# Kernel optimization log

Hardware: AMD Instinct MI355X
Metric: run time of the kernel (lower is better)

Reference implementation:

```python
import jax, jax.numpy as jnp
import numpy as np

# Dims from HierarchicalDecoder defaults; NB is the torch batch size, which the
# original code accidentally uses as the LSTM time axis (2D input to nn.LSTM).
Z_DIM, U, COND, HID, OUT, NB = 512, 16, 512, 1024, 16, 512


def _unif(key, shape, scale):
    return jax.random.uniform(key, shape, jnp.float32, -scale, scale)


def setup_inputs() -> dict:
    key = jax.random.key(0)
    ks = jax.random.split(key, 20)
    d = Z_DIM // U            # 32
    sd = 1.0 / np.sqrt(d)
    sc = 1.0 / np.sqrt(COND)
    sh = 1.0 / np.sqrt(HID)
    return {
        "z": jax.random.normal(ks[0], (NB, Z_DIM), jnp.float32),
        "fc0_w": _unif(ks[1], (COND, d), sd), "fc0_b": _unif(ks[2], (COND,), sd),
        "fc1_w": _unif(ks[3], (HID, COND), sc), "fc1_b": _unif(ks[4], (HID,), sc),
        # conductor LSTM (2 layers, input=hidden=COND); b = b_ih + b_hh fused
        "c_wih0": _unif(ks[5], (4 * COND, COND), sc), "c_whh0": _unif(ks[6], (4 * COND, COND), sc), "c_b0": _unif(ks[7], (4 * COND,), sc),
        "c_wih1": _unif(ks[8], (4 * COND, COND), sc), "c_whh1": _unif(ks[9], (4 * COND, COND), sc), "c_b1": _unif(ks[10], (4 * COND,), sc),
        # decoder LSTM (2 layers, input COND->HID then HID->HID)
        "d_wih0": _unif(ks[11], (4 * HID, COND), sh), "d_whh0": _unif(ks[12], (4 * HID, HID), sh), "d_b0": _unif(ks[13], (4 * HID,), sh),
        "d_wih1": _unif(ks[14], (4 * HID, HID), sh), "d_whh1": _unif(ks[15], (4 * HID, HID), sh), "d_b1": _unif(ks[16], (4 * HID,), sh),
        "out_w": _unif(ks[17], (OUT, HID), sh), "out_b": _unif(ks[18], (OUT,), sh),
    }


def _lstm_layer(x, h0, c0, wih, whh, b):
    # x: [U, T, I]; h0, c0: [U, H]. PyTorch gate order: i, f, g, o.
    gx = jnp.einsum('uti,gi->utg', x, wih) + b  # input contribution, hoisted out of scan

    def step(carry, g):
        h, c = carry
        g = g + h @ whh.T
        i, f, gg, o = jnp.split(g, 4, axis=-1)
        c = jax.nn.sigmoid(f) * c + jax.nn.sigmoid(i) * jnp.tanh(gg)
        h = jax.nn.sigmoid(o) * jnp.tanh(c)
        return (h, c), h

    (hT, _), hs = jax.lax.scan(step, (h0, c0), jnp.swapaxes(gx, 0, 1))
    return jnp.swapaxes(hs, 0, 1), hT  # [U, T, H], [U, H]


def _forward(z, fc0_w, fc0_b, fc1_w, fc1_b, c_wih0, c_whh0, c_b0, c_wih1, c_whh1, c_b1,
             d_wih0, d_whh0, d_b0, d_wih1, d_whh1, d_b1, out_w, out_b):
    B = z.shape[0]
    # [U, B, z_dim//U]; the Python loop over U in the original is vectorized as a batch axis.
    x = jnp.swapaxes(z.reshape(B, U, -1), 0, 1)
    x = jnp.tanh(x @ fc0_w.T + fc0_b)  # fc0 -> [U, B, COND]; B is the LSTM time axis
    zC = jnp.zeros((U, COND), x.dtype)
    h0s, hT0 = _lstm_layer(x, zC, zC, c_wih0, c_whh0, c_b0)
    h1s, hT1 = _lstm_layer(h0s, zC, zC, c_wih1, c_whh1, c_b1)
    # fc1 on final conductor hidden of each layer -> decoder initial h; initial c = 0
    hd0 = jnp.tanh(hT0 @ fc1_w.T + fc1_b)
    hd1 = jnp.tanh(hT1 @ fc1_w.T + fc1_b)
    zH = jnp.zeros((U, HID), x.dtype)
    d0s, _ = _lstm_layer(h1s, hd0, zH, d_wih0, d_whh0, d_b0)
    d1s, _ = _lstm_layer(d0s, hd1, zH, d_wih1, d_whh1, d_b1)
    logits = d1s @ out_w.T + out_b                 # [U, B, OUT]
    probs = jax.nn.softmax(logits, axis=1)         # Softmax(dim=0) over the B axis per subsequence
    return jnp.swapaxes(probs, 0, 1).reshape(B, U * OUT)  # torch.cat(outputs, dim=1)


def reference(z, fc0_w, fc0_b, fc1_w, fc1_b, c_wih0, c_whh0, c_b0, c_wih1, c_whh1, c_b1,
              d_wih0, d_whh0, d_b0, d_wih1, d_whh1, d_b1, out_w, out_b):
    return _forward(z, fc0_w, fc0_b, fc1_w, fc1_b, c_wih0, c_whh0, c_b0, c_wih1, c_whh1, c_b1,
                    d_wih0, d_whh0, d_b0, d_wih1, d_whh1, d_b1, out_w, out_b)
```

## Files before the change

### kernel.cpp

```cpp
#include <hip/hip_runtime.h>
#include <hip/hip_bf16.h>
#include <cstdio>


typedef __attribute__((ext_vector_type(8))) short short8;
typedef __attribute__((ext_vector_type(4))) float f32x4;
typedef __attribute__((ext_vector_type(2))) unsigned int u32x2;
using bf16 = __hip_bfloat16;

__device__ __forceinline__ float bfraw2f(short s){
  return __uint_as_float(((unsigned)(unsigned short)s) << 16);
}
__device__ __forceinline__ unsigned bfbits(float f){
  __hip_bfloat16 h = __float2bfloat16(f);
  return (unsigned)*reinterpret_cast<unsigned short*>(&h);
}

__device__ __forceinline__ void gbar_arrive(unsigned* flags, unsigned gen){
  asm volatile("s_waitcnt vmcnt(0)" ::: "memory");
  __syncthreads();
  if (threadIdx.x == 0)
    __hip_atomic_store(&flags[blockIdx.x], gen,
                       __ATOMIC_RELAXED, __HIP_MEMORY_SCOPE_AGENT);
}
template<int BASE, int N>
__device__ __forceinline__ void lead_wait_pub(const unsigned* flags, unsigned* wm8,
                                              unsigned gen){
  if (threadIdx.x < 64){
    const int l = threadIdx.x;
    for (;;){
      bool ok = true;
#pragma unroll
      for (int k = 0; k < (N + 63) / 64; ++k){
        int idx = l + k * 64;
        if (idx < N)
          ok &= (__hip_atomic_load(&flags[BASE + idx], __ATOMIC_RELAXED,
                                   __HIP_MEMORY_SCOPE_AGENT) >= gen);
      }
      if (__all(ok)) break;
    }
    if (l < 8)
      __hip_atomic_store(&wm8[l * 16], gen, __ATOMIC_RELAXED,
                         __HIP_MEMORY_SCOPE_AGENT);
  }
  __syncthreads();
}
__device__ __forceinline__ void worker_wait(const unsigned* wm8, unsigned gen){
  if (threadIdx.x == 0){
    const unsigned* p = &wm8[(blockIdx.x & 7) * 16];
    while (__hip_atomic_load(p, __ATOMIC_RELAXED, __HIP_MEMORY_SCOPE_AGENT) < gen)
      __builtin_amdgcn_s_sleep(1);
  }
  __syncthreads();
}

template<int N>
__device__ __forceinline__ void ldA(const bf16* base, short8* av){
#pragma unroll
  for (int i = 0; i < N; ++i)
    av[i] = *(const short8*)(base + i * 32);
}
__device__ __forceinline__ void vm0(){
  asm volatile("s_waitcnt vmcnt(0)" ::: "memory");
  __builtin_amdgcn_sched_barrier(0);
}

__device__ __forceinline__ void gate_tile(const float v[4], float* c_st,
                                          int col, int kg, int jb,
                                          bf16* hrow, int Hl, float* hTrow)
{
  const int g = col & 3;
#pragma unroll
  for (int rr = 0; rr < 4; ++rr){
    float a = (g == 2) ? tanhf(v[rr]) : 1.f / (1.f + expf(-v[rr]));
    float x1 = __shfl_xor(a, 1);
    float x2 = __shfl_xor(a, 2);
    float x3 = __shfl_xor(x1, 2);
    float cn = x1 * c_st[rr] + a * x2;
    float hn = x3 * tanhf(cn);
    c_st[rr] = cn;
    float h4 = __shfl_xor(hn, 4), h8 = __shfl_xor(hn, 8), h12 = __shfl_xor(hn, 12);
    if (col == 0){
      int u = kg * 4 + rr;
      u32x2 pk;
      pk.x = bfbits(hn) | (bfbits(h4) << 16);
      pk.y = bfbits(h8) | (bfbits(h12) << 16);
      bf16* p = hrow + (size_t)u * Hl + jb;
      asm volatile("global_store_dwordx2 %0, %1, off sc0 sc1"
                   :: "v"(p), "v"(pk) : "memory");
      if (hTrow){
        f32x4 hv = {hn, h4, h8, h12};
        *(f32x4*)(hTrow + (size_t)u * Hl + jb) = hv;
      }
    }
  }
}

__global__ void k_prep_w(const float* __restrict__ srcA, const float* __restrict__ srcB,
                         int K1, int K2, int H, bf16* __restrict__ dst)
{
  const int row = blockIdx.x;
  const int j = row >> 2, g = row & 3;
  const int Kt = K1 + K2;
  const float* sA = srcA + (size_t)(g * H + j) * K1;
  const float* sB = srcB ? srcB + (size_t)(g * H + j) * K2 : nullptr;
  bf16* d = dst + (size_t)row * Kt;
  for (int k = threadIdx.x; k < Kt; k += blockDim.x)
    d[k] = __float2bfloat16(k < K1 ? sA[k] : sB[k - K1]);
}

__global__ void k_prep_b(const float* __restrict__ src, int H, float* __restrict__ dst){
  int i = blockIdx.x * blockDim.x + threadIdx.x;
  if (i < 4 * H) dst[i] = src[(i & 3) * H + (i >> 2)];
}

__global__ void k_conv_bf(const float* __restrict__ src, bf16* __restrict__ dst, int n){
  int i = blockIdx.x * blockDim.x + threadIdx.x;
  if (i < n) dst[i] = __float2bfloat16(src[i]);
}

__global__ void k_fc0(const float* __restrict__ z, const float* __restrict__ w,
                      const float* __restrict__ b, bf16* __restrict__ x)
{
  const int m = blockIdx.x;
  const int t = m >> 4, u = m & 15;
  const float* zr = z + (size_t)t * 512 + u * 32;
  float zv[32];
#pragma unroll
  for (int k = 0; k < 32; ++k) zv[k] = zr[k];
  for (int n = threadIdx.x; n < 512; n += 256){
    const float* wr = w + n * 32;
    float s = b[n];
#pragma unroll
    for (int k = 0; k < 32; ++k) s += zv[k] * wr[k];
    x[(size_t)m * 512 + n] = __float2bfloat16(tanhf(s));
  }
}

__device__ __forceinline__ void gload16(const void* g, void* lds_wave_base){
  __builtin_amdgcn_global_load_lds((const __attribute__((address_space(1))) void*)g,
                                   (__attribute__((address_space(3))) void*)lds_wave_base,
                                   16, 0, 0);
}

__global__ __launch_bounds__(256) void k_gemm_gx0(const bf16* __restrict__ A,
                                                  const bf16* __restrict__ W,
                                                  const float* __restrict__ bias,
                                                  float* __restrict__ C)
{
  __shared__ bf16 Al[128 * 64];
  __shared__ bf16 Bl[128 * 64];
  const int tid = threadIdx.x, lane = tid & 63, wave = tid >> 6;
  const int bm = blockIdx.x & 63, bn = blockIdx.x >> 6;
  const int wm = wave >> 1, wn = wave & 1;
  const int col = lane & 15, kg = lane >> 4;

  f32x4 acc[4][4];
#pragma unroll
  for (int i = 0; i < 4; ++i)
#pragma unroll
    for (int q = 0; q < 4; ++q) acc[i][q] = f32x4{0.f, 0.f, 0.f, 0.f};

  const int r = tid >> 3, c8 = (tid & 7) * 8;
  for (int k0 = 0; k0 < 512; k0 += 64){
    const bf16* ga = A + (size_t)(bm * 128 + r) * 512 + k0 + c8;
    const bf16* gb = W + (size_t)(bn * 128 + r) * 512 + k0 + c8;
#pragma unroll
    for (int i = 0; i < 4; ++i){
      gload16(ga + (size_t)32 * i * 512, (char*)Al + (size_t)i * 4096 + wave * 1024);
      gload16(gb + (size_t)32 * i * 512, (char*)Bl + (size_t)i * 4096 + wave * 1024);
    }
    __syncthreads();
#pragma unroll
    for (int kb = 0; kb < 2; ++kb){
      short8 af[4], bfr[4];
#pragma unroll
      for (int i = 0; i < 4; ++i)
        af[i] = *(const short8*)&Al[(wm * 64 + i * 16 + col) * 64 + kb * 32 + kg * 8];
#pragma unroll
      for (int i = 0; i < 4; ++i)
        bfr[i] = *(const short8*)&Bl[(wn * 64 + i * 16 + col) * 64 + kb * 32 + kg * 8];
#pragma unroll
      for (int i = 0; i < 4; ++i)
#pragma unroll
        for (int q = 0; q < 4; ++q)
          acc[i][q] = __builtin_amdgcn_mfma_f32_16x16x32_bf16(af[i], bfr[q], acc[i][q], 0, 0, 0);
    }
    __syncthreads();
  }
#pragma unroll
  for (int i = 0; i < 4; ++i)
#pragma unroll
    for (int q = 0; q < 4; ++q){
      int cc = bn * 128 + wn * 64 + q * 16 + col;
      float bv = bias[cc];
#pragma unroll
      for (int rr = 0; rr < 4; ++rr){
        int rrow = bm * 128 + wm * 64 + i * 16 + kg * 4 + rr;
        C[(size_t)rrow * 2048 + cc] = acc[i][q][rr] + bv;
      }
    }
}

__global__ __launch_bounds__(512, 2) void k_cond(
    const bf16* __restrict__ Wc0, const bf16* __restrict__ Wc1,
    const float* __restrict__ bc1, const float* __restrict__ gx0,
    bf16* h0seq, bf16* h1seq, float* hT0, float* hT1,
    unsigned* flags, unsigned* wm)
{
  const int wg = blockIdx.x, tid = threadIdx.x;
  const int lane = tid & 63, wave = tid >> 6;
  const int col = lane & 15, kg = lane >> 4;
  const int r = col;
  const bool L0 = wg < 16;
  unsigned* wm0 = wm;
  unsigned* wm1 = wm + 128;
  __shared__ f32x4 part[4][64];

  int tileIdx, half = 0;
  if (L0) tileIdx = wg * 8 + wave;
  else  { tileIdx = (wg - 16) * 4 + (wave >> 1); half = wave & 1; }
  const int colp = tileIdx * 16 + col;
  const int jb = tileIdx * 4;

  short8 breg[16];
  {
    const bf16* W = L0 ? (Wc0 + (size_t)colp * 512)
                       : (Wc1 + (size_t)colp * 1024 + half * 512);
#pragma unroll
    for (int i = 0; i < 16; ++i) breg[i] = *(const short8*)(W + i * 32 + kg * 8);
  }
#pragma unroll
  for (int i = 0; i < 16; ++i) asm volatile("" : "+v"(breg[i]));

  const float bias = L0 ? 0.f : bc1[colp];
  float c_st[4] = {0.f, 0.f, 0.f, 0.f};
  f32x4 acc_pre = {0.f, 0.f, 0.f, 0.f};
  float gxv[4];
  if (L0){
#pragma unroll
    for (int rr = 0; rr < 4; ++rr)
      gxv[rr] = gx0[((size_t)(kg * 4 + rr)) * 2048 + colp];
  }

  for (int tick = 0; tick < 513; ++tick){
    const int t = tick - (L0 ? 0 : 1);
    const bool active = (t >= 0 && t < 512);
    f32x4 acc = {0.f, 0.f, 0.f, 0.f};
    if (active){
      if (L0){
        short8 av[16];
        ldA<16>(h0seq + (size_t)t * 8192 + r * 512 + kg * 8, av);
        vm0();
#pragma unroll
        for (int i = 0; i < 16; ++i)
          acc = __builtin_amdgcn_mfma_f32_16x16x32_bf16(av[i], breg[i], acc, 0, 0, 0);
      } else if (half == 0){
        acc = acc_pre;
      } else {
        short8 av[16];
        ldA<16>(h1seq + (size_t)t * 8192 + r * 512 + kg * 8, av);
        vm0();
#pragma unroll
        for (int i = 0; i < 16; ++i)
          acc = __builtin_amdgcn_mfma_f32_16x16x32_bf16(av[i], breg[i], acc, 0, 0, 0);
        part[wave >> 1][lane] = acc;
      }
    }
    if (!L0) __syncthreads();
    if (active && (L0 || half == 0)){
      float v[4];
      if (L0){
#pragma unroll
        for (int rr = 0; rr < 4; ++rr) v[rr] = acc[rr] + gxv[rr];
      } else {
        f32x4 p2 = part[wave >> 1][lane];
#pragma unroll
        for (int rr = 0; rr < 4; ++rr) v[rr] = acc[rr] + p2[rr] + bias;
      }
      bf16* hrow = (L0 ? h0seq : h1seq) + (size_t)(t + 1) * 8192;
      float* hTp = (t == 511) ? (L0 ? hT0 : hT1) : nullptr;
      gate_tile(v, c_st, col, kg, jb, hrow, 512, hTp);
    }
    gbar_arrive(flags, (unsigned)(tick + 1));
    if (L0){
      if (tick + 1 < 512){
#pragma unroll
        for (int rr = 0; rr < 4; ++rr)
          gxv[rr] = gx0[((size_t)(tick + 1) * 16 + kg * 4 + rr) * 2048 + colp];
      }
      if (wg == 0) lead_wait_pub<0, 16>(flags, wm0, (unsigned)(tick + 1));
      else         worker_wait(wm0, (unsigned)(tick + 1));
    } else {
      if (tick < 512){
        worker_wait(wm0, (unsigned)(tick + 1));
        if (half == 0){
          short8 av[16];
          ldA<16>(h0seq + (size_t)(tick + 1) * 8192 + r * 512 + kg * 8, av);
          vm0();
          acc_pre = f32x4{0.f, 0.f, 0.f, 0.f};
#pragma unroll
          for (int i = 0; i < 16; ++i)
            acc_pre = __builtin_amdgcn_mfma_f32_16x16x32_bf16(av[i], breg[i], acc_pre, 0, 0, 0);
        }
      }
      if (wg == 16) lead_wait_pub<16, 32>(flags, wm1, (unsigned)(tick + 1));
      else          worker_wait(wm1, (unsigned)(tick + 1));
    }
  }
}

__global__ void k_hd(const float* __restrict__ hT0, const float* __restrict__ hT1,
                     const float* __restrict__ w, const float* __restrict__ b,
                     bf16* __restrict__ d0s0, bf16* __restrict__ d1s0)
{
  int gid = blockIdx.x * 256 + threadIdx.x;
  int sel = gid >> 14;
  int u = (gid >> 10) & 15, n = gid & 1023;
  const float* h = (sel ? hT1 : hT0) + u * 512;
  const float* wr = w + (size_t)n * 512;
  float s = b[n];
  for (int k = 0; k < 512; ++k) s += h[k] * wr[k];
  (sel ? d1s0 : d0s0)[(size_t)u * 1024 + n] = __float2bfloat16(tanhf(s));
}

__global__ __launch_bounds__(512, 2) void k_dec(
    const bf16* __restrict__ Wd0, const bf16* __restrict__ Wd1,
    const float* __restrict__ bd0, const float* __restrict__ bd1,
    const bf16* __restrict__ h1seq, bf16* d0seq, bf16* d1seq,
    unsigned* flags, unsigned* wm)
{
  const int wg = blockIdx.x, tid = threadIdx.x;
  const int lane = tid & 63, wave = tid >> 6;
  const int col = lane & 15, kg = lane >> 4, r = col;
  const bool L0 = wg < 128;
  const int grp = wave >> 2, q = wave & 3;
  const int tileIdx = (L0 ? wg : wg - 128) * 2 + grp;
  const int colp = tileIdx * 16 + col;
  const int jb = tileIdx * 4;
  unsigned* wm0 = wm;
  unsigned* wm1 = wm + 128;
  __shared__ f32x4 part[2][3][64];

  short8 breg[16];
#pragma unroll
  for (int i = 0; i < 16; ++i) breg[i] = short8{0,0,0,0,0,0,0,0};
  if (L0){
    const bf16* W = Wd0 + (size_t)colp * 1536 + q * 384;
#pragma unroll
    for (int i = 0; i < 12; ++i) breg[i] = *(const short8*)(W + i * 32 + kg * 8);
  } else {
    const bf16* W = Wd1 + (size_t)colp * 2048 + q * 512;
#pragma unroll
    for (int i = 0; i < 16; ++i) breg[i] = *(const short8*)(W + i * 32 + kg * 8);
  }
#pragma unroll
  for (int i = 0; i < 16; ++i) asm volatile("" : "+v"(breg[i]));

  const float bias = L0 ? bd0[colp] : bd1[colp];
  float c_st[4] = {0.f, 0.f, 0.f, 0.f};
  f32x4 acc_pre = {0.f, 0.f, 0.f, 0.f};

  if (L0){
    if (q == 0){
      short8 av[12];
      ldA<12>(h1seq + (size_t)1 * 8192 + r * 512 + kg * 8, av);
      vm0();
#pragma unroll
      for (int i = 0; i < 12; ++i)
        acc_pre = __builtin_amdgcn_mfma_f32_16x16x32_bf16(av[i], breg[i], acc_pre, 0, 0, 0);
    } else if (q == 1){
      short8 av[4];
      ldA<4>(h1seq + (size_t)1 * 8192 + r * 512 + kg * 8 + 384, av);
      vm0();
#pragma unroll
      for (int i = 0; i < 4; ++i)
        acc_pre = __builtin_amdgcn_mfma_f32_16x16x32_bf16(av[i], breg[i], acc_pre, 0, 0, 0);
    }
  }

  for (int tick = 0; tick < 513; ++tick){
    const int t = tick - (L0 ? 0 : 1);
    const bool active = (t >= 0 && t < 512);
    f32x4 acc = {0.f, 0.f, 0.f, 0.f};
    if (active){
      short8 av[16];
      if (L0){
        const bf16* d0p = d0seq + (size_t)t * 16384 + r * 1024 + kg * 8;
        if      (q == 0)  acc = acc_pre;
        else if (q == 1){
          ldA<8>(d0p, av);
          vm0();
          acc = acc_pre;
#pragma unroll
          for (int i = 0; i < 8; ++i)
            acc = __builtin_amdgcn_mfma_f32_16x16x32_bf16(av[i], breg[4 + i], acc, 0, 0, 0);
        } else {
          ldA<12>(d0p + (q == 2 ? 256 : 640), av);
          vm0();
#pragma unroll
          for (int i = 0; i < 12; ++i)
            acc = __builtin_amdgcn_mfma_f32_16x16x32_bf16(av[i], breg[i], acc, 0, 0, 0);
        }
      } else {
        if (q < 2){
          acc = acc_pre;
        } else {
          const bf16* d1c = d1seq + (size_t)t * 16384 + r * 1024 + kg * 8;
          ldA<16>(d1c + (q == 3 ? 512 : 0), av);
          vm0();
#pragma unroll
          for (int i = 0; i < 16; ++i)
            acc = __builtin_amdgcn_mfma_f32_16x16x32_bf16(av[i], breg[i], acc, 0, 0, 0);
        }
      }
      if (q != 0) part[grp][q - 1][lane] = acc;
    }
    __syncthreads();
    if (active && q == 0){
      f32x4 p0 = part[grp][0][lane], p1 = part[grp][1][lane], p2 = part[grp][2][lane];
      float v[4];
#pragma unroll
      for (int rr = 0; rr < 4; ++rr) v[rr] = acc[rr] + p0[rr] + p1[rr] + p2[rr] + bias;
      bf16* hrow = (L0 ? d0seq : d1seq) + (size_t)(t + 1) * 16384;
      gate_tile(v, c_st, col, kg, jb, hrow, 1024, nullptr);
    }
    gbar_arrive(flags, (unsigned)(tick + 1));
    if (L0){
      if (tick + 1 < 512){
        if (q == 0){
          short8 av[12];
          ldA<12>(h1seq + (size_t)(tick + 2) * 8192 + r * 512 + kg * 8, av);
          vm0();
          acc_pre = f32x4{0.f, 0.f, 0.f, 0.f};
#pragma unroll
          for (int i = 0; i < 12; ++i)
            acc_pre = __builtin_amdgcn_mfma_f32_16x16x32_bf16(av[i], breg[i], acc_pre, 0, 0, 0);
        } else if (q == 1){
          short8 av[4];
          ldA<4>(h1seq + (size_t)(tick + 2) * 8192 + r * 512 + kg * 8 + 384, av);
          vm0();
          acc_pre = f32x4{0.f, 0.f, 0.f, 0.f};
#pragma unroll
          for (int i = 0; i < 4; ++i)
            acc_pre = __builtin_amdgcn_mfma_f32_16x16x32_bf16(av[i], breg[i], acc_pre, 0, 0, 0);
        }
      }
      if (wg == 0) lead_wait_pub<0, 128>(flags, wm0, (unsigned)(tick + 1));
      else         worker_wait(wm0, (unsigned)(tick + 1));
    } else {
      if (tick < 512){
        worker_wait(wm0, (unsigned)(tick + 1));
        if (q < 2){
          short8 av[16];
          ldA<16>(d0seq + (size_t)(tick + 1) * 16384 + r * 1024 + kg * 8 + q * 512, av);
          vm0();
          acc_pre = f32x4{0.f, 0.f, 0.f, 0.f};
#pragma unroll
          for (int i = 0; i < 16; ++i)
            acc_pre = __builtin_amdgcn_mfma_f32_16x16x32_bf16(av[i], breg[i], acc_pre, 0, 0, 0);
        }
      }
      if (wg == 128) lead_wait_pub<128, 128>(flags, wm1, (unsigned)(tick + 1));
      else           worker_wait(wm1, (unsigned)(tick + 1));
    }
  }
}

__global__ __launch_bounds__(256) void k_logits(const bf16* __restrict__ d1seq,
                                                const bf16* __restrict__ ow,
                                                const float* __restrict__ ob,
                                                float* __restrict__ logits)
{
  const int u = blockIdx.x >> 4, tb = blockIdx.x & 15;
  __shared__ bf16 rows[32][1024];
  const int tid = threadIdx.x;
  for (int idx = tid; idx < 4096; idx += 256){
    int tl = idx >> 7, seg = idx & 127;
    *(short8*)&rows[tl][seg * 8] =
      *(const short8*)(d1seq + ((size_t)(tb * 32 + tl + 1) * 16 + u) * 1024 + seg * 8);
  }
  __syncthreads();
  for (int p = tid; p < 512; p += 256){
    int tl = p >> 4, o = p & 15;
    const bf16* wr = ow + (size_t)o * 1024;
    float s = 0.f;
    for (int k = 0; k < 1024; k += 8){
      short8 av = *(const short8*)&rows[tl][k];
      short8 wv = *(const short8*)(wr + k);
#pragma unroll
      for (int e = 0; e < 8; ++e) s += bfraw2f(av[e]) * bfraw2f(wv[e]);
    }
    logits[((size_t)u * 16 + o) * 512 + tb * 32 + tl] = s + ob[o];
  }
}

__global__ __launch_bounds__(256) void k_softmax(const float* __restrict__ logits,
                                                 float* __restrict__ out)
{
  const int u = blockIdx.x >> 4, o = blockIdx.x & 15;
  const float* L = logits + ((size_t)u * 16 + o) * 512;
  const int tid = threadIdx.x;
  float v0 = L[tid], v1 = L[tid + 256];
  float m = fmaxf(v0, v1);
  for (int d = 1; d < 64; d <<= 1) m = fmaxf(m, __shfl_xor(m, d));
  __shared__ float red[4], red2[4];
  if ((tid & 63) == 0) red[tid >> 6] = m;
  __syncthreads();
  m = fmaxf(fmaxf(red[0], red[1]), fmaxf(red[2], red[3]));
  float e0 = expf(v0 - m), e1 = expf(v1 - m);
  float s = e0 + e1;
  for (int d = 1; d < 64; d <<= 1) s += __shfl_xor(s, d);
  if ((tid & 63) == 0) red2[tid >> 6] = s;
  __syncthreads();
  s = red2[0] + red2[1] + red2[2] + red2[3];
  float inv = 1.f / s;
  out[(size_t)tid * 256 + u * 16 + o] = e0 * inv;
  out[(size_t)(tid + 256) * 256 + u * 16 + o] = e1 * inv;
}

extern "C" void kernel_launch(void* const* d_in, const int* in_sizes, int n_in,
                              void* d_out, int out_size, void* d_ws, size_t ws_size,
                              hipStream_t stream)
{
  const float* z      = (const float*)d_in[0];
  const float* fc0_w  = (const float*)d_in[1];
  const float* fc0_b  = (const float*)d_in[2];
  const float* fc1_w  = (const float*)d_in[3];
  const float* fc1_b  = (const float*)d_in[4];
  const float* c_wih0 = (const float*)d_in[5];
  const float* c_whh0 = (const float*)d_in[6];
  const float* c_b0   = (const float*)d_in[7];
  const float* c_wih1 = (const float*)d_in[8];
  const float* c_whh1 = (const float*)d_in[9];
  const float* c_b1   = (const float*)d_in[10];
  const float* d_wih0 = (const float*)d_in[11];
  const float* d_whh0 = (const float*)d_in[12];
  const float* d_b0   = (const float*)d_in[13];
  const float* d_wih1 = (const float*)d_in[14];
  const float* d_whh1 = (const float*)d_in[15];
  const float* d_b1   = (const float*)d_in[16];
  const float* out_w  = (const float*)d_in[17];
  const float* out_b  = (const float*)d_in[18];

  char* p = (char*)d_ws;
  auto alloc = [&](size_t bytes) -> char* {
    char* r = p; p += (bytes + 255) & ~(size_t)255; return r;
  };
  bf16*  Wgx0p  = (bf16*)alloc(2048ull * 512 * 2);
  bf16*  Wc0p   = (bf16*)alloc(2048ull * 512 * 2);
  bf16*  Wc1p   = (bf16*)alloc(2048ull * 1024 * 2);
  bf16*  Wd0p   = (bf16*)alloc(4096ull * 1536 * 2);
  bf16*  Wd1p   = (bf16*)alloc(4096ull * 2048 * 2);
  float* bc0p   = (float*)alloc(2048 * 4);
  float* bc1p   = (float*)alloc(2048 * 4);
  float* bd0p   = (float*)alloc(4096 * 4);
  float* bd1p   = (float*)alloc(4096 * 4);
  bf16*  outwbf = (bf16*)alloc(16384 * 2);
  bf16*  x      = (bf16*)alloc(8192ull * 512 * 2);
  float* gx0    = (float*)alloc(8192ull * 2048 * 4);
  bf16*  h0seq  = (bf16*)alloc(513ull * 16 * 512 * 2);
  bf16*  h1seq  = (bf16*)alloc(513ull * 16 * 512 * 2);
  bf16*  d0seq  = (bf16*)alloc(513ull * 16 * 1024 * 2);
  bf16*  d1seq  = (bf16*)alloc(513ull * 16 * 1024 * 2);
  float* hT0    = (float*)alloc(16 * 512 * 4);
  float* hT1    = (float*)alloc(16 * 512 * 4);
  float* logits = (float*)alloc(16ull * 16 * 512 * 4);
  unsigned* flagC = (unsigned*)alloc(64 * 4);
  unsigned* flagD = (unsigned*)alloc(256 * 4);
  unsigned* wmC   = (unsigned*)alloc(1024);
  unsigned* wmD   = (unsigned*)alloc(1024);
  if ((size_t)(p - (char*)d_ws) > ws_size){
    fprintf(stderr, "kernel_launch: ws too small (%zu needed, %zu given)\n",
            (size_t)(p - (char*)d_ws), ws_size);
    return;
  }

  hipMemsetAsync(flagC, 0, 64 * 4, stream);
  hipMemsetAsync(flagD, 0, 256 * 4, stream);
  hipMemsetAsync(wmC, 0, 1024, stream);
  hipMemsetAsync(wmD, 0, 1024, stream);
  hipMemsetAsync(h0seq, 0, 16 * 512 * 2, stream);
  hipMemsetAsync(h1seq, 0, 16 * 512 * 2, stream);

  k_prep_w<<<2048, 256, 0, stream>>>(c_wih0, nullptr, 512, 0,   512, Wgx0p);
  k_prep_w<<<2048, 256, 0, stream>>>(c_whh0, nullptr, 512, 0,   512, Wc0p);
  k_prep_w<<<2048, 256, 0, stream>>>(c_wih1, c_whh1, 512, 512,  512, Wc1p);
  k_prep_w<<<4096, 256, 0, stream>>>(d_wih0, d_whh0, 512, 1024, 1024, Wd0p);
  k_prep_w<<<4096, 256, 0, stream>>>(d_wih1, d_whh1, 1024, 1024, 1024, Wd1p);
  k_prep_b<<<8,  256, 0, stream>>>(c_b0, 512,  bc0p);
  k_prep_b<<<8,  256, 0, stream>>>(c_b1, 512,  bc1p);
  k_prep_b<<<16, 256, 0, stream>>>(d_b0, 1024, bd0p);
  k_prep_b<<<16, 256, 0, stream>>>(d_b1, 1024, bd1p);
  k_conv_bf<<<64, 256, 0, stream>>>(out_w, outwbf, 16 * 1024);

  k_fc0<<<8192, 256, 0, stream>>>(z, fc0_w, fc0_b, x);
  k_gemm_gx0<<<1024, 256, 0, stream>>>(x, Wgx0p, bc0p, gx0);

  k_cond<<<48, 512, 0, stream>>>(Wc0p, Wc1p, bc1p, gx0, h0seq, h1seq, hT0, hT1, flagC, wmC);
  k_hd<<<128, 256, 0, stream>>>(hT0, hT1, fc1_w, fc1_b, d0seq, d1seq);
  k_dec<<<256, 512, 0, stream>>>(Wd0p, Wd1p, bd0p, bd1p, h1seq, d0seq, d1seq, flagD, wmD);

  k_logits<<<256, 256, 0, stream>>>(d1seq, outwbf, out_b, logits);
  k_softmax<<<256, 256, 0, stream>>>(logits, (float*)d_out);
}
```

Before: 6.850 ms.

## Shrink conductor LSTM to 24 blocks with direct flag polling instead of leader relay

Layer 0 of the conductor now uses 8 workgroups, each wave computing two gate tiles. Layer 1 uses 16 workgroups, each wave holding the full 1024-wide weight slice in registers, which removes the LDS partial-sum exchange and its __syncthreads. The two-level leader/worker barrier is replaced by every block polling all peer flags directly, and the s_sleep in worker_wait is removed. This cuts per-step barrier latency and the number of participating blocks, at the cost of more registers per wave (occupancy bound drops to 1), more per-wave serial MFMA work, and more polling traffic.

```diff
diff --git a/kernel.cpp b/kernel.cpp
--- a/kernel.cpp
+++ b/kernel.cpp
@@ -22,6 +22,20 @@
   if (threadIdx.x == 0)
     __hip_atomic_store(&flags[blockIdx.x], gen,
                        __ATOMIC_RELAXED, __HIP_MEMORY_SCOPE_AGENT);
+}
+template<int BASE, int N>
+__device__ __forceinline__ void dpoll(const unsigned* flags, unsigned gen){
+  if (threadIdx.x < 64){
+    const int l = threadIdx.x;
+    for (;;){
+      unsigned v = 0xFFFFFFFFu;
+      if (l < N)
+        v = __hip_atomic_load(&flags[BASE + l], __ATOMIC_RELAXED,
+                              __HIP_MEMORY_SCOPE_AGENT);
+      if (__all(v >= gen)) break;
+    }
+  }
+  __syncthreads();
 }
 template<int BASE, int N>
 __device__ __forceinline__ void lead_wait_pub(const unsigned* flags, unsigned* wm8,
@@ -49,7 +63,7 @@
   if (threadIdx.x == 0){
     const unsigned* p = &wm8[(blockIdx.x & 7) * 16];
     while (__hip_atomic_load(p, __ATOMIC_RELAXED, __HIP_MEMORY_SCOPE_AGENT) < gen)
-      __builtin_amdgcn_s_sleep(1);
+      ;
   }
   __syncthreads();
 }
@@ -202,110 +216,114 @@
     }
 }
 
-__global__ __launch_bounds__(512, 2) void k_cond(
+__global__ __launch_bounds__(512, 1) void k_cond(
     const bf16* __restrict__ Wc0, const bf16* __restrict__ Wc1,
     const float* __restrict__ bc1, const float* __restrict__ gx0,
-    bf16* h0seq, bf16* h1seq, float* hT0, float* hT1,
-    unsigned* flags, unsigned* wm)
+    bf16* h0seq, bf16* h1seq, float* hT0, float* hT1, unsigned* flags)
 {
   const int wg = blockIdx.x, tid = threadIdx.x;
   const int lane = tid & 63, wave = tid >> 6;
-  const int col = lane & 15, kg = lane >> 4;
-  const int r = col;
-  const bool L0 = wg < 16;
-  unsigned* wm0 = wm;
-  unsigned* wm1 = wm + 128;
-  __shared__ f32x4 part[4][64];
-
-  int tileIdx, half = 0;
-  if (L0) tileIdx = wg * 8 + wave;
-  else  { tileIdx = (wg - 16) * 4 + (wave >> 1); half = wave & 1; }
-  const int colp = tileIdx * 16 + col;
-  const int jb = tileIdx * 4;
-
-  short8 breg[16];
-  {
-    const bf16* W = L0 ? (Wc0 + (size_t)colp * 512)
-                       : (Wc1 + (size_t)colp * 1024 + half * 512);
-#pragma unroll
-    for (int i = 0; i < 16; ++i) breg[i] = *(const short8*)(W + i * 32 + kg * 8);
-  }
-#pragma unroll
-  for (int i = 0; i < 16; ++i) asm volatile("" : "+v"(breg[i]));
-
-  const float bias = L0 ? 0.f : bc1[colp];
-  float c_st[4] = {0.f, 0.f, 0.f, 0.f};
-  f32x4 acc_pre = {0.f, 0.f, 0.f, 0.f};
-  float gxv[4];
-  if (L0){
-#pragma unroll
-    for (int rr = 0; rr < 4; ++rr)
-      gxv[rr] = gx0[((size_t)(kg * 4 + rr)) * 2048 + colp];
-  }
-
-  for (int tick = 0; tick < 513; ++tick){
-    const int t = tick - (L0 ? 0 : 1);
-    const bool active = (t >= 0 && t < 512);
-    f32x4 acc = {0.f, 0.f, 0.f, 0.f};
-    if (active){
-      if (L0){
+  const int col = lane & 15, kg = lane >> 4, r = col;
+
+  if (wg < 8){
+    const int gw = wg * 8 + wave;
+    int colp[2], jb[2];
+#pragma unroll
+    for (int p = 0; p < 2; ++p){ colp[p] = (gw * 2 + p) * 16 + col; jb[p] = (gw * 2 + p) * 4; }
+
+    short8 breg[2][16];
+#pragma unroll
+    for (int p = 0; p < 2; ++p)
+#pragma unroll
+      for (int i = 0; i < 16; ++i)
+        breg[p][i] = *(const short8*)(Wc0 + (size_t)colp[p] * 512 + i * 32 + kg * 8);
+#pragma unroll
+    for (int p = 0; p < 2; ++p)
+#pragma unroll
+      for (int i = 0; i < 16; ++i) asm volatile("" : "+v"(breg[p][i]));
+
+    float c_st[2][4] = {{0.f,0.f,0.f,0.f},{0.f,0.f,0.f,0.f}};
+    float gxv[2][4];
+#pragma unroll
+    for (int p = 0; p < 2; ++p)
+#pragma unroll
+      for (int rr = 0; rr < 4; ++rr)
+        gxv[p][rr] = gx0[((size_t)(kg * 4 + rr)) * 2048 + colp[p]];
+
+    for (int tick = 0; tick < 513; ++tick){
+      const int t = tick;
+      if (t < 512){
         short8 av[16];
         ldA<16>(h0seq + (size_t)t * 8192 + r * 512 + kg * 8, av);
         vm0();
-#pragma unroll
-        for (int i = 0; i < 16; ++i)
-          acc = __builtin_amdgcn_mfma_f32_16x16x32_bf16(av[i], breg[i], acc, 0, 0, 0);
-      } else if (half == 0){
-        acc = acc_pre;
-      } else {
+        f32x4 a0 = {0.f,0.f,0.f,0.f}, a1 = {0.f,0.f,0.f,0.f};
+#pragma unroll
+        for (int i = 0; i < 16; ++i){
+          a0 = __builtin_amdgcn_mfma_f32_16x16x32_bf16(av[i], breg[0][i], a0, 0, 0, 0);
+          a1 = __builtin_amdgcn_mfma_f32_16x16x32_bf16(av[i], breg[1][i], a1, 0, 0, 0);
+        }
+        bf16* hrow = h0seq + (size_t)(t + 1) * 8192;
+        float* hTp = (t == 511) ? hT0 : nullptr;
+        float v0[4], v1[4];
+#pragma unroll
+        for (int rr = 0; rr < 4; ++rr){ v0[rr] = a0[rr] + gxv[0][rr]; v1[rr] = a1[rr] + gxv[1][rr]; }
+        gate_tile(v0, c_st[0], col, kg, jb[0], hrow, 512, hTp);
+        gate_tile(v1, c_st[1], col, kg, jb[1], hrow, 512, hTp);
+      }
+      gbar_arrive(flags, (unsigned)(tick + 1));
+      if (tick + 1 < 512){
+#pragma unroll
+        for (int p = 0; p < 2; ++p)
+#pragma unroll
+          for (int rr = 0; rr < 4; ++rr)
+            gxv[p][rr] = gx0[((size_t)(tick + 1) * 16 + kg * 4 + rr) * 2048 + colp[p]];
+      }
+      dpoll<0, 8>(flags, (unsigned)(tick + 1));
+    }
+  } else {
+    const int gw = (wg - 8) * 8 + wave;
+    const int colp = gw * 16 + col;
+    const int jb = gw * 4;
+
+    short8 breg[32];
+#pragma unroll
+    for (int i = 0; i < 32; ++i)
+      breg[i] = *(const short8*)(Wc1 + (size_t)colp * 1024 + i * 32 + kg * 8);
+#pragma unroll
+    for (int i = 0; i < 32; ++i) asm volatile("" : "+v"(breg[i]));
+
+    const float bias = bc1[colp];
+    float c_st[4] = {0.f, 0.f, 0.f, 0.f};
+    f32x4 acc_pre = {0.f, 0.f, 0.f, 0.f};
+
+    for (int tick = 0; tick < 513; ++tick){
+      const int t = tick - 1;
+      if (t >= 0){
         short8 av[16];
         ldA<16>(h1seq + (size_t)t * 8192 + r * 512 + kg * 8, av);
         vm0();
+        f32x4 acc = acc_pre;
 #pragma unroll
         for (int i = 0; i < 16; ++i)
-          acc = __builtin_amdgcn_mfma_f32_16x16x32_bf16(av[i], breg[i], acc, 0, 0, 0);
-        part[wave >> 1][lane] = acc;
-      }
-    }
-    if (!L0) __syncthreads();
-    if (active && (L0 || half == 0)){
-      float v[4];
-      if (L0){
-#pragma unroll
-        for (int rr = 0; rr < 4; ++rr) v[rr] = acc[rr] + gxv[rr];
-      } else {
-        f32x4 p2 = part[wave >> 1][lane];
-#pragma unroll
-        for (int rr = 0; rr < 4; ++rr) v[rr] = acc[rr] + p2[rr] + bias;
-      }
-      bf16* hrow = (L0 ? h0seq : h1seq) + (size_t)(t + 1) * 8192;
-      float* hTp = (t == 511) ? (L0 ? hT0 : hT1) : nullptr;
-      gate_tile(v, c_st, col, kg, jb, hrow, 512, hTp);
-    }
-    gbar_arrive(flags, (unsigned)(tick + 1));
-    if (L0){
-      if (tick + 1 < 512){
-#pragma unroll
-        for (int rr = 0; rr < 4; ++rr)
-          gxv[rr] = gx0[((size_t)(tick + 1) * 16 + kg * 4 + rr) * 2048 + colp];
-      }
-      if (wg == 0) lead_wait_pub<0, 16>(flags, wm0, (unsigned)(tick + 1));
-      else         worker_wait(wm0, (unsigned)(tick + 1));
-    } else {
+          acc = __builtin_amdgcn_mfma_f32_16x16x32_bf16(av[i], breg[16 + i], acc, 0, 0, 0);
+        float v[4];
+#pragma unroll
+        for (int rr = 0; rr < 4; ++rr) v[rr] = acc[rr] + bias;
+        float* hTp = (t == 511) ? hT1 : nullptr;
+        gate_tile(v, c_st, col, kg, jb, h1seq + (size_t)(t + 1) * 8192, 512, hTp);
+      }
+      gbar_arrive(flags, (unsigned)(tick + 1));
       if (tick < 512){
-        worker_wait(wm0, (unsigned)(tick + 1));
-        if (half == 0){
-          short8 av[16];
-          ldA<16>(h0seq + (size_t)(tick + 1) * 8192 + r * 512 + kg * 8, av);
-          vm0();
-          acc_pre = f32x4{0.f, 0.f, 0.f, 0.f};
-#pragma unroll
-          for (int i = 0; i < 16; ++i)
-            acc_pre = __builtin_amdgcn_mfma_f32_16x16x32_bf16(av[i], breg[i], acc_pre, 0, 0, 0);
-        }
-      }
-      if (wg == 16) lead_wait_pub<16, 32>(flags, wm1, (unsigned)(tick + 1));
-      else          worker_wait(wm1, (unsigned)(tick + 1));
+        dpoll<0, 8>(flags, (unsigned)(tick + 1));
+        short8 av[16];
+        ldA<16>(h0seq + (size_t)(tick + 1) * 8192 + r * 512 + kg * 8, av);
+        vm0();
+        acc_pre = f32x4{0.f, 0.f, 0.f, 0.f};
+#pragma unroll
+        for (int i = 0; i < 16; ++i)
+          acc_pre = __builtin_amdgcn_mfma_f32_16x16x32_bf16(av[i], breg[i], acc_pre, 0, 0, 0);
+      }
+      dpoll<8, 16>(flags, (unsigned)(tick + 1));
     }
   }
 }
@@ -568,7 +586,6 @@
   float* logits = (float*)alloc(16ull * 16 * 512 * 4);
   unsigned* flagC = (unsigned*)alloc(64 * 4);
   unsigned* flagD = (unsigned*)alloc(256 * 4);
-  unsigned* wmC   = (unsigned*)alloc(1024);
   unsigned* wmD   = (unsigned*)alloc(1024);
   if ((size_t)(p - (char*)d_ws) > ws_size){
     fprintf(stderr, "kernel_launch: ws too small (%zu needed, %zu given)\n",
@@ -578,7 +595,6 @@
 
   hipMemsetAsync(flagC, 0, 64 * 4, stream);
   hipMemsetAsync(flagD, 0, 256 * 4, stream);
-  hipMemsetAsync(wmC, 0, 1024, stream);
   hipMemsetAsync(wmD, 0, 1024, stream);
   hipMemsetAsync(h0seq, 0, 16 * 512 * 2, stream);
   hipMemsetAsync(h1seq, 0, 16 * 512 * 2, stream);
@@ -597,7 +613,7 @@
   k_fc0<<<8192, 256, 0, stream>>>(z, fc0_w, fc0_b, x);
   k_gemm_gx0<<<1024, 256, 0, stream>>>(x, Wgx0p, bc0p, gx0);
 
-  k_cond<<<48, 512, 0, stream>>>(Wc0p, Wc1p, bc1p, gx0, h0seq, h1seq, hT0, hT1, flagC, wmC);
+  k_cond<<<24, 512, 0, stream>>>(Wc0p, Wc1p, bc1p, gx0, h0seq, h1seq, hT0, hT1, flagC);
   k_hd<<<128, 256, 0, stream>>>(hT0, hT1, fc1_w, fc1_b, d0seq, d1seq);
   k_dec<<<256, 512, 0, stream>>>(Wd0p, Wd1p, bd0p, bd1p, h1seq, d0seq, d1seq, flagD, wmD);
 
```

Measured after the change: 8.375 ms. 1.22x slower.
